# Optimization experiments

Measured on AMD Instinct MI355X. Metric: run time of the kernel, lower is better.

Reference implementation:

```python
import jax, jax.numpy as jnp
import numpy as np

N_NODES = 50000
N_EDGES = 800000
IN_DIM, HID_DIM, OUT_DIM = 128, 256, 64


def setup_inputs() -> dict:
    key = jax.random.key(0)
    k1, k2, k3, k4 = jax.random.split(key, 4)
    x = jax.random.normal(k1, (N_NODES, IN_DIM), dtype=jnp.float32)
    edge_index = jax.random.randint(k2, (2, N_EDGES), 0, N_NODES, dtype=jnp.int32)
    # Glorot-ish scaled weights
    W1 = jax.random.normal(k3, (IN_DIM, HID_DIM), dtype=jnp.float32) * (1.0 / np.sqrt(IN_DIM))
    W2 = jax.random.normal(k4, (HID_DIM, OUT_DIM), dtype=jnp.float32) * (1.0 / np.sqrt(HID_DIM))
    b1 = jnp.zeros((HID_DIM,), dtype=jnp.float32)
    b2 = jnp.zeros((OUT_DIM,), dtype=jnp.float32)
    return {"x": x, "edge_index": edge_index, "W1": W1, "b1": b1, "W2": W2, "b2": b2}


def _gcn_conv(x, src, dst, deg_inv_sqrt, W, b):
    # transform first (PyG GCNConv order), then edge-normalized scatter-add
    h = x @ W                                        # [N, D_out]
    norm = deg_inv_sqrt[src] * deg_inv_sqrt[dst]     # [E]
    msgs = h[src] * norm[:, None]                    # [E, D_out]
    agg = jax.ops.segment_sum(msgs, dst, num_segments=x.shape[0])
    return agg + b


def reference(x, edge_index, W1, b1, W2, b2):
    n = x.shape[0]
    loops = jnp.arange(n, dtype=edge_index.dtype)
    src = jnp.concatenate([edge_index[0], loops])    # add self-loops
    dst = jnp.concatenate([edge_index[1], loops])
    deg = jax.ops.segment_sum(jnp.ones_like(dst, dtype=x.dtype), dst, num_segments=n)
    deg_inv_sqrt = jnp.where(deg > 0, jax.lax.rsqrt(jnp.maximum(deg, 1e-12)), 0.0)
    h = jax.nn.relu(_gcn_conv(x, src, dst, deg_inv_sqrt, W1, b1))
    h = _gcn_conv(h, src, dst, deg_inv_sqrt, W2, b2)
    return jax.nn.log_softmax(h, axis=1)
```

## Files before the change

kernel.cpp:

```cpp
#include <hip/hip_runtime.h>
#include <hip/hip_bf16.h>
#include <math.h>

#define N_NODES 50000
#define N_EDGES 800000
#define IN_DIM 128
#define HID_DIM 256
#define OUT_DIM 64
#define NPART 196
#define CHUNK 2048
#define NPB ((N_EDGES + CHUNK - 1) / CHUNK)
#define PREPB (N_NODES * IN_DIM / 4 / 256)

typedef __attribute__((ext_vector_type(8))) short bf16x8;
typedef __attribute__((ext_vector_type(4))) short short4v;
typedef __attribute__((ext_vector_type(4))) float f32x4;

__device__ inline short f2bf(float f) {
    unsigned u = __float_as_uint(f);
    unsigned r = (u + 0x7fffu + ((u >> 16) & 1u)) >> 16;
    return (short)r;
}
__device__ inline float bf_lo(unsigned u) { return __uint_as_float(u << 16); }
__device__ inline float bf_hi(unsigned u) { return __uint_as_float(u & 0xffff0000u); }

__global__ void hist_kernel(const int* __restrict__ dst, int* __restrict__ cnt, int E) {
    int e = blockIdx.x * blockDim.x + threadIdx.x;
    if (e < E) atomicAdd(&cnt[dst[e]], 1);
}

__global__ __launch_bounds__(256) void scan_pack_kernel(const int* __restrict__ cnt,
                                                        int* __restrict__ offs,
                                                        float* __restrict__ dis,
                                                        int* __restrict__ gcnt,
                                                        int* __restrict__ coarseBase,
                                                        int* __restrict__ coarseCnt,
                                                        int* __restrict__ coarseCursor,
                                                        const float* __restrict__ W1,
                                                        const float* __restrict__ W2,
                                                        short* __restrict__ Bp1,
                                                        short* __restrict__ Bp2, int n) {
    if (blockIdx.x >= NPART) {
        int idx = (blockIdx.x - NPART) * 256 + threadIdx.x;
        const float* W; short* Bp; int N;
        const int T1 = (IN_DIM / 32) * (HID_DIM / 16) * 64;
        const int T2 = (HID_DIM / 32) * (OUT_DIM / 16) * 64;
        if (idx < T1) { W = W1; Bp = Bp1; N = HID_DIM; }
        else { idx -= T1; if (idx >= T2) return; W = W2; Bp = Bp2; N = OUT_DIM; }
        int lane = idx & 63;
        int frag = idx >> 6;
        int ntiles = N >> 4;
        int nt = frag % ntiles;
        int kt = frag / ntiles;
        int col = nt * 16 + (lane & 15);
        int krow = kt * 32 + (lane >> 4) * 8;
        bf16x8 pk;
        #pragma unroll
        for (int j = 0; j < 8; j++) pk[j] = f2bf(W[(size_t)(krow + j) * N + col]);
        *((bf16x8*)(Bp + (size_t)idx * 8)) = pk;
        return;
    }
    __shared__ int ws[4];
    __shared__ int base;
    int tid = threadIdx.x, lane = tid & 63, wid = tid >> 6;
    int i = blockIdx.x * 256 + tid;
    int v = (i < n) ? cnt[i] : 0;
    int s = v;
    #pragma unroll
    for (int off = 1; off < 64; off <<= 1) {
        int t = __shfl_up(s, off, 64);
        if (lane >= off) s += t;
    }
    if (lane == 63) ws[wid] = s;
    __syncthreads();
    int wp = 0;
    #pragma unroll
    for (int w = 0; w < 4; w++) wp += (w < wid) ? ws[w] : 0;
    int excl = s - v + wp;
    if (tid == 255) {
        int total = excl + v;
        int b = atomicAdd(gcnt, total);
        base = b;
        coarseBase[blockIdx.x] = b;
        coarseCnt[blockIdx.x] = total;
        coarseCursor[blockIdx.x] = b;
    }
    __syncthreads();
    if (i < n) {
        offs[i] = base + excl;
        dis[i] = rsqrtf((float)v + 1.0f);
    }
}

__global__ __launch_bounds__(256) void part1_prep_kernel(const int* __restrict__ src,
                                                         const int* __restrict__ dst,
                                                         int* __restrict__ coarseCursor,
                                                         uint2* __restrict__ sedge,
                                                         const float* __restrict__ x,
                                                         const float* __restrict__ dis,
                                                         short* __restrict__ xb, int E) {
    __shared__ int cnt_l[NPART];
    __shared__ int pref[NPART];
    __shared__ int gbase[NPART];
    __shared__ int ws4[4];
    __shared__ uint2 stage[CHUNK];
    int tid = threadIdx.x;
    if (blockIdx.x >= NPB) {
        int idx = (blockIdx.x - NPB) * 256 + tid;
        int node = idx >> 5;
        float dn = dis[node];
        float4 v = ((const float4*)x)[idx];
        short4v o = {f2bf(v.x * dn), f2bf(v.y * dn), f2bf(v.z * dn), f2bf(v.w * dn)};
        ((short4v*)xb)[idx] = o;
        return;
    }
    int e0 = blockIdx.x * CHUNK;
    if (tid < NPART) cnt_l[tid] = 0;
    __syncthreads();
    int es[CHUNK / 256], ed[CHUNK / 256];
    #pragma unroll
    for (int j = 0; j < CHUNK / 256; j++) {
        int e = e0 + j * 256 + tid;
        if (e < E) {
            es[j] = src[e]; ed[j] = dst[e];
            atomicAdd(&cnt_l[ed[j] >> 8], 1);
        } else ed[j] = -1;
    }
    __syncthreads();
    int lane = tid & 63, wid = tid >> 6;
    int v = (tid < NPART) ? cnt_l[tid] : 0;
    int s = v;
    #pragma unroll
    for (int off = 1; off < 64; off <<= 1) {
        int t = __shfl_up(s, off, 64);
        if (lane >= off) s += t;
    }
    if (lane == 63) ws4[wid] = s;
    __syncthreads();
    int wp = 0;
    #pragma unroll
    for (int w = 0; w < 4; w++) wp += (w < wid) ? ws4[w] : 0;
    int excl = s - v + wp;
    if (tid < NPART) pref[tid] = excl;
    __syncthreads();
    if (tid < NPART) cnt_l[tid] = excl;
    __syncthreads();
    #pragma unroll
    for (int j = 0; j < CHUNK / 256; j++) {
        if (ed[j] >= 0) {
            int c = ed[j] >> 8;
            int p = atomicAdd(&cnt_l[c], 1);
            stage[p] = make_uint2((unsigned)es[j], (unsigned)ed[j]);
        }
    }
    __syncthreads();
    if (tid < NPART) {
        int cl = cnt_l[tid] - pref[tid];
        gbase[tid] = (cl > 0) ? atomicAdd(&coarseCursor[tid], cl) : 0;
    }
    __syncthreads();
    int total = (e0 + CHUNK <= E) ? CHUNK : (E - e0);
    for (int i = tid; i < total; i += 256) {
        uint2 ev = stage[i];
        int c = (int)(ev.y >> 8);
        sedge[gbase[c] + (i - pref[c])] = ev;
    }
}

__global__ __launch_bounds__(256) void part2_kernel(const uint2* __restrict__ sedge,
                                                    const int* __restrict__ coarseBase,
                                                    const int* __restrict__ coarseCnt,
                                                    const int* __restrict__ offs,
                                                    int* __restrict__ ssrc, int n) {
    __shared__ int cur[256];
    int b = blockIdx.x;
    int node0 = b * 256;
    int tid = threadIdx.x;
    if (node0 + tid < n) cur[tid] = offs[node0 + tid];
    __syncthreads();
    int base = coarseBase[b], cb = coarseCnt[b];
    for (int i = tid; i < cb; i += 256) {
        uint2 ev = sedge[base + i];
        int pos = atomicAdd(&cur[ev.y & 255], 1);
        ssrc[pos] = (int)ev.x;
    }
}

__global__ void agg1_kernel(const short* __restrict__ xb, const int* __restrict__ ssrc,
                            const int* __restrict__ offs, const int* __restrict__ cnt,
                            const float* __restrict__ dis, short* __restrict__ aggx, int n) {
    int lane = threadIdx.x & 63;
    int node = blockIdx.x * (blockDim.x >> 6) + (threadIdx.x >> 6);
    if (node >= n) return;
    int grp = lane >> 4, l16 = lane & 15;
    int start = offs[node], c = cnt[node];
    float acc[8] = {};
    int j = grp;
    for (; j + 12 < c; j += 16) {
        int s0 = ssrc[start + j];
        int s1 = ssrc[start + j + 4];
        int s2 = ssrc[start + j + 8];
        int s3 = ssrc[start + j + 12];
        uint4 p0 = *((const uint4*)(xb + (size_t)s0 * IN_DIM + l16 * 8));
        uint4 p1 = *((const uint4*)(xb + (size_t)s1 * IN_DIM + l16 * 8));
        uint4 p2 = *((const uint4*)(xb + (size_t)s2 * IN_DIM + l16 * 8));
        uint4 p3 = *((const uint4*)(xb + (size_t)s3 * IN_DIM + l16 * 8));
        acc[0] += bf_lo(p0.x); acc[1] += bf_hi(p0.x); acc[2] += bf_lo(p0.y); acc[3] += bf_hi(p0.y);
        acc[4] += bf_lo(p0.z); acc[5] += bf_hi(p0.z); acc[6] += bf_lo(p0.w); acc[7] += bf_hi(p0.w);
        acc[0] += bf_lo(p1.x); acc[1] += bf_hi(p1.x); acc[2] += bf_lo(p1.y); acc[3] += bf_hi(p1.y);
        acc[4] += bf_lo(p1.z); acc[5] += bf_hi(p1.z); acc[6] += bf_lo(p1.w); acc[7] += bf_hi(p1.w);
        acc[0] += bf_lo(p2.x); acc[1] += bf_hi(p2.x); acc[2] += bf_lo(p2.y); acc[3] += bf_hi(p2.y);
        acc[4] += bf_lo(p2.z); acc[5] += bf_hi(p2.z); acc[6] += bf_lo(p2.w); acc[7] += bf_hi(p2.w);
        acc[0] += bf_lo(p3.x); acc[1] += bf_hi(p3.x); acc[2] += bf_lo(p3.y); acc[3] += bf_hi(p3.y);
        acc[4] += bf_lo(p3.z); acc[5] += bf_hi(p3.z); acc[6] += bf_lo(p3.w); acc[7] += bf_hi(p3.w);
    }
    for (; j < c; j += 4) {
        int s0 = ssrc[start + j];
        uint4 p0 = *((const uint4*)(xb + (size_t)s0 * IN_DIM + l16 * 8));
        acc[0] += bf_lo(p0.x); acc[1] += bf_hi(p0.x); acc[2] += bf_lo(p0.y); acc[3] += bf_hi(p0.y);
        acc[4] += bf_lo(p0.z); acc[5] += bf_hi(p0.z); acc[6] += bf_lo(p0.w); acc[7] += bf_hi(p0.w);
    }
    #pragma unroll
    for (int k = 0; k < 8; k++) {
        acc[k] += __shfl_xor(acc[k], 16, 64);
        acc[k] += __shfl_xor(acc[k], 32, 64);
    }
    if (grp == 0) {
        float dn = dis[node];
        uint4 pk = *((const uint4*)(xb + (size_t)node * IN_DIM + l16 * 8));
        acc[0] += bf_lo(pk.x); acc[1] += bf_hi(pk.x); acc[2] += bf_lo(pk.y); acc[3] += bf_hi(pk.y);
        acc[4] += bf_lo(pk.z); acc[5] += bf_hi(pk.z); acc[6] += bf_lo(pk.w); acc[7] += bf_hi(pk.w);
        bf16x8 o;
        #pragma unroll
        for (int k = 0; k < 8; k++) o[k] = f2bf(acc[k] * dn);
        *((bf16x8*)(aggx + (size_t)node * IN_DIM + l16 * 8)) = o;
    }
}

#define H1_STRIDE 264
__global__ __launch_bounds__(256) void gemm_fused_kernel(const short* __restrict__ A,
                                                         const short* __restrict__ Bp1,
                                                         const short* __restrict__ Bp2,
                                                         const float* __restrict__ b1,
                                                         const float* __restrict__ dis,
                                                         short* __restrict__ h2, int M) {
    __shared__ short lds_h1[4][16][H1_STRIDE];
    int lane = threadIdx.x & 63;
    int w = threadIdx.x >> 6;
    int rowBase = blockIdx.x * 64 + w * 16;
    int arow = rowBase + (lane & 15);
    int kseg = lane >> 4;
    int col0 = lane & 15;

    constexpr int NT1 = HID_DIM / 16;
    f32x4 acc1[NT1] = {};
    #pragma unroll
    for (int kt = 0; kt < IN_DIM / 32; kt++) {
        bf16x8 a = {};
        if (arow < M)
            a = *((const bf16x8*)(A + (size_t)arow * IN_DIM + kt * 32 + kseg * 8));
        #pragma unroll
        for (int nt = 0; nt < NT1; nt++) {
            bf16x8 b = *((const bf16x8*)(Bp1 + ((size_t)(kt * NT1 + nt) * 64 + lane) * 8));
            acc1[nt] = __builtin_amdgcn_mfma_f32_16x16x32_bf16(a, b, acc1[nt], 0, 0, 0);
        }
    }
    #pragma unroll
    for (int nt = 0; nt < NT1; nt++) {
        float bv = b1[nt * 16 + col0];
        #pragma unroll
        for (int i = 0; i < 4; i++) {
            float v = fmaxf(acc1[nt][i] + bv, 0.0f);
            lds_h1[w][kseg * 4 + i][nt * 16 + col0] = f2bf(v);
        }
    }
    constexpr int NT2 = OUT_DIM / 16;
    f32x4 acc2[NT2] = {};
    #pragma unroll
    for (int kt = 0; kt < HID_DIM / 32; kt++) {
        bf16x8 a = *((const bf16x8*)&lds_h1[w][lane & 15][kt * 32 + kseg * 8]);
        #pragma unroll
        for (int nt = 0; nt < NT2; nt++) {
            bf16x8 b = *((const bf16x8*)(Bp2 + ((size_t)(kt * NT2 + nt) * 64 + lane) * 8));
            acc2[nt] = __builtin_amdgcn_mfma_f32_16x16x32_bf16(a, b, acc2[nt], 0, 0, 0);
        }
    }
    #pragma unroll
    for (int i = 0; i < 4; i++) {
        int r = rowBase + kseg * 4 + i;
        if (r >= M) continue;
        float sc = dis[r];
        #pragma unroll
        for (int nt = 0; nt < NT2; nt++)
            h2[(size_t)r * OUT_DIM + nt * 16 + col0] = f2bf(acc2[nt][i] * sc);
    }
}

__global__ void agg2_kernel(const short* __restrict__ h2, const int* __restrict__ ssrc,
                            const int* __restrict__ offs, const int* __restrict__ cnt,
                            const float* __restrict__ dis, const float* __restrict__ b2,
                            float* __restrict__ out, int n) {
    int lane = threadIdx.x & 63;
    int node = blockIdx.x * (blockDim.x >> 6) + (threadIdx.x >> 6);
    if (node >= n) return;
    int grp = lane >> 4, l16 = lane & 15;
    int start = offs[node], c = cnt[node];
    float acc[4] = {};
    int j = grp;
    for (; j + 12 < c; j += 16) {
        int s0 = ssrc[start + j];
        int s1 = ssrc[start + j + 4];
        int s2 = ssrc[start + j + 8];
        int s3 = ssrc[start + j + 12];
        uint2 p0 = *((const uint2*)(h2 + (size_t)s0 * OUT_DIM + l16 * 4));
        uint2 p1 = *((const uint2*)(h2 + (size_t)s1 * OUT_DIM + l16 * 4));
        uint2 p2 = *((const uint2*)(h2 + (size_t)s2 * OUT_DIM + l16 * 4));
        uint2 p3 = *((const uint2*)(h2 + (size_t)s3 * OUT_DIM + l16 * 4));
        acc[0] += bf_lo(p0.x); acc[1] += bf_hi(p0.x); acc[2] += bf_lo(p0.y); acc[3] += bf_hi(p0.y);
        acc[0] += bf_lo(p1.x); acc[1] += bf_hi(p1.x); acc[2] += bf_lo(p1.y); acc[3] += bf_hi(p1.y);
        acc[0] += bf_lo(p2.x); acc[1] += bf_hi(p2.x); acc[2] += bf_lo(p2.y); acc[3] += bf_hi(p2.y);
        acc[0] += bf_lo(p3.x); acc[1] += bf_hi(p3.x); acc[2] += bf_lo(p3.y); acc[3] += bf_hi(p3.y);
    }
    for (; j < c; j += 4) {
        int s0 = ssrc[start + j];
        uint2 p0 = *((const uint2*)(h2 + (size_t)s0 * OUT_DIM + l16 * 4));
        acc[0] += bf_lo(p0.x); acc[1] += bf_hi(p0.x); acc[2] += bf_lo(p0.y); acc[3] += bf_hi(p0.y);
    }
    #pragma unroll
    for (int k = 0; k < 4; k++) {
        acc[k] += __shfl_xor(acc[k], 16, 64);
        acc[k] += __shfl_xor(acc[k], 32, 64);
    }
    float dn = dis[node];
    uint2 pv = *((const uint2*)(h2 + (size_t)node * OUT_DIM + l16 * 4));
    float4 bb = ((const float4*)b2)[l16];
    acc[0] = (acc[0] + bf_lo(pv.x)) * dn + bb.x;
    acc[1] = (acc[1] + bf_hi(pv.x)) * dn + bb.y;
    acc[2] = (acc[2] + bf_lo(pv.y)) * dn + bb.z;
    acc[3] = (acc[3] + bf_hi(pv.y)) * dn + bb.w;
    float m = fmaxf(fmaxf(acc[0], acc[1]), fmaxf(acc[2], acc[3]));
    #pragma unroll
    for (int off = 1; off < 16; off <<= 1) m = fmaxf(m, __shfl_xor(m, off, 64));
    float ex = expf(acc[0] - m) + expf(acc[1] - m) + expf(acc[2] - m) + expf(acc[3] - m);
    #pragma unroll
    for (int off = 1; off < 16; off <<= 1) ex += __shfl_xor(ex, off, 64);
    float ls = m + logf(ex);
    if (grp == 0) {
        float4 o = {acc[0] - ls, acc[1] - ls, acc[2] - ls, acc[3] - ls};
        ((float4*)(out + (size_t)node * OUT_DIM))[l16] = o;
    }
}

extern "C" void kernel_launch(void* const* d_in, const int* in_sizes, int n_in,
                              void* d_out, int out_size, void* d_ws, size_t ws_size,
                              hipStream_t stream) {
    const float* x  = (const float*)d_in[0];
    const int*   ei = (const int*)d_in[1];
    const float* W1 = (const float*)d_in[2];
    const float* b1 = (const float*)d_in[3];
    const float* W2 = (const float*)d_in[4];
    const float* b2 = (const float*)d_in[5];
    float* out = (float*)d_out;
    char* ws = (char*)d_ws;

    const int* srcp = ei;
    const int* dstp = ei + N_EDGES;

    int*   cnt    = (int*)(ws);
    int*   gcnt   = (int*)(ws + 200000);
    int*   offs   = (int*)(ws + 262144);
    float* dis    = (float*)(ws + 524288);
    int*   coarseBase   = (int*)(ws + 786432);
    int*   coarseCnt    = (int*)(ws + 787456);
    int*   coarseCursor = (int*)(ws + 788480);
    short* Bp1    = (short*)(ws + 1048576);
    short* Bp2    = (short*)(ws + 1114112);
    int*   ssrc   = (int*)(ws + 1179648);
    uint2* sedge  = (uint2*)(ws + 4456448);
    short* aggx   = (short*)(ws + 4456448);
    short* xb     = (short*)(ws + 17301504);
    short* h2     = (short*)(ws + 30146560);

    hipMemsetAsync(cnt, 0, 200004, stream);

    hist_kernel<<<(N_EDGES + 255) / 256, 256, 0, stream>>>(dstp, cnt, N_EDGES);
    scan_pack_kernel<<<NPART + 24, 256, 0, stream>>>(cnt, offs, dis, gcnt,
                                                     coarseBase, coarseCnt, coarseCursor,
                                                     W1, W2, Bp1, Bp2, N_NODES);
    part1_prep_kernel<<<NPB + PREPB, 256, 0, stream>>>(srcp, dstp, coarseCursor, sedge,
                                                       x, dis, xb, N_EDGES);
    part2_kernel<<<NPART, 256, 0, stream>>>(sedge, coarseBase, coarseCnt, offs, ssrc, N_NODES);

    agg1_kernel<<<(N_NODES + 3) / 4, 256, 0, stream>>>(xb, ssrc, offs, cnt, dis, aggx, N_NODES);
    gemm_fused_kernel<<<(N_NODES + 63) / 64, 256, 0, stream>>>(aggx, Bp1, Bp2, b1, dis,
                                                               h2, N_NODES);
    agg2_kernel<<<(N_NODES + 3) / 4, 256, 0, stream>>>(h2, ssrc, offs, cnt, dis, b2, out, N_NODES);
}
```

Baseline: 228.3 us.

## Drop global histogram pass; bucket edges into fixed-capacity coarse partitions

Removes the global degree histogram and scan kernels. Edges are bucketed straight into fixed-capacity (CAP) slots per 256-node partition, and part2 then computes per-node counts, offsets and degree norms locally. The x-to-bf16 scaling also moves into part2, which cuts two launches and a pass over dst. The risk is that a coarse partition holding more than CAP edges would overflow; random uniform inputs average about 4096 per partition, and the ssrc layout gains gaps.

```diff
diff --git a/kernel.cpp b/kernel.cpp
--- a/kernel.cpp
+++ b/kernel.cpp
@@ -8,9 +8,9 @@
 #define HID_DIM 256
 #define OUT_DIM 64
 #define NPART 196
+#define CAP 8192
 #define CHUNK 2048
 #define NPB ((N_EDGES + CHUNK - 1) / CHUNK)
-#define PREPB (N_NODES * IN_DIM / 4 / 256)
 
 typedef __attribute__((ext_vector_type(8))) short bf16x8;
 typedef __attribute__((ext_vector_type(4))) short short4v;
@@ -24,24 +24,22 @@
 __device__ inline float bf_lo(unsigned u) { return __uint_as_float(u << 16); }
 __device__ inline float bf_hi(unsigned u) { return __uint_as_float(u & 0xffff0000u); }
 
-__global__ void hist_kernel(const int* __restrict__ dst, int* __restrict__ cnt, int E) {
-    int e = blockIdx.x * blockDim.x + threadIdx.x;
-    if (e < E) atomicAdd(&cnt[dst[e]], 1);
-}
-
-__global__ __launch_bounds__(256) void scan_pack_kernel(const int* __restrict__ cnt,
-                                                        int* __restrict__ offs,
-                                                        float* __restrict__ dis,
-                                                        int* __restrict__ gcnt,
-                                                        int* __restrict__ coarseBase,
-                                                        int* __restrict__ coarseCnt,
-                                                        int* __restrict__ coarseCursor,
-                                                        const float* __restrict__ W1,
-                                                        const float* __restrict__ W2,
-                                                        short* __restrict__ Bp1,
-                                                        short* __restrict__ Bp2, int n) {
-    if (blockIdx.x >= NPART) {
-        int idx = (blockIdx.x - NPART) * 256 + threadIdx.x;
+__global__ __launch_bounds__(256) void part1_pack_kernel(const int* __restrict__ src,
+                                                         const int* __restrict__ dst,
+                                                         int* __restrict__ coarseCursor,
+                                                         uint2* __restrict__ sedge,
+                                                         const float* __restrict__ W1,
+                                                         const float* __restrict__ W2,
+                                                         short* __restrict__ Bp1,
+                                                         short* __restrict__ Bp2, int E) {
+    __shared__ int cnt_l[NPART];
+    __shared__ int pref[NPART];
+    __shared__ int gbase[NPART];
+    __shared__ int ws4[4];
+    __shared__ uint2 stage[CHUNK];
+    int tid = threadIdx.x;
+    if (blockIdx.x >= NPB) {
+        int idx = (blockIdx.x - NPB) * 256 + tid;
         const float* W; short* Bp; int N;
         const int T1 = (IN_DIM / 32) * (HID_DIM / 16) * 64;
         const int T2 = (HID_DIM / 32) * (OUT_DIM / 16) * 64;
@@ -60,60 +58,6 @@
         *((bf16x8*)(Bp + (size_t)idx * 8)) = pk;
         return;
     }
-    __shared__ int ws[4];
-    __shared__ int base;
-    int tid = threadIdx.x, lane = tid & 63, wid = tid >> 6;
-    int i = blockIdx.x * 256 + tid;
-    int v = (i < n) ? cnt[i] : 0;
-    int s = v;
-    #pragma unroll
-    for (int off = 1; off < 64; off <<= 1) {
-        int t = __shfl_up(s, off, 64);
-        if (lane >= off) s += t;
-    }
-    if (lane == 63) ws[wid] = s;
-    __syncthreads();
-    int wp = 0;
-    #pragma unroll
-    for (int w = 0; w < 4; w++) wp += (w < wid) ? ws[w] : 0;
-    int excl = s - v + wp;
-    if (tid == 255) {
-        int total = excl + v;
-        int b = atomicAdd(gcnt, total);
-        base = b;
-        coarseBase[blockIdx.x] = b;
-        coarseCnt[blockIdx.x] = total;
-        coarseCursor[blockIdx.x] = b;
-    }
-    __syncthreads();
-    if (i < n) {
-        offs[i] = base + excl;
-        dis[i] = rsqrtf((float)v + 1.0f);
-    }
-}
-
-__global__ __launch_bounds__(256) void part1_prep_kernel(const int* __restrict__ src,
-                                                         const int* __restrict__ dst,
-                                                         int* __restrict__ coarseCursor,
-                                                         uint2* __restrict__ sedge,
-                                                         const float* __restrict__ x,
-                                                         const float* __restrict__ dis,
-                                                         short* __restrict__ xb, int E) {
-    __shared__ int cnt_l[NPART];
-    __shared__ int pref[NPART];
-    __shared__ int gbase[NPART];
-    __shared__ int ws4[4];
-    __shared__ uint2 stage[CHUNK];
-    int tid = threadIdx.x;
-    if (blockIdx.x >= NPB) {
-        int idx = (blockIdx.x - NPB) * 256 + tid;
-        int node = idx >> 5;
-        float dn = dis[node];
-        float4 v = ((const float4*)x)[idx];
-        short4v o = {f2bf(v.x * dn), f2bf(v.y * dn), f2bf(v.z * dn), f2bf(v.w * dn)};
-        ((short4v*)xb)[idx] = o;
-        return;
-    }
     int e0 = blockIdx.x * CHUNK;
     if (tid < NPART) cnt_l[tid] = 0;
     __syncthreads();
@@ -156,7 +100,7 @@
     __syncthreads();
     if (tid < NPART) {
         int cl = cnt_l[tid] - pref[tid];
-        gbase[tid] = (cl > 0) ? atomicAdd(&coarseCursor[tid], cl) : 0;
+        gbase[tid] = (cl > 0) ? (tid * CAP + atomicAdd(&coarseCursor[tid], cl)) : 0;
     }
     __syncthreads();
     int total = (e0 + CHUNK <= E) ? CHUNK : (E - e0);
@@ -168,21 +112,65 @@
 }
 
 __global__ __launch_bounds__(256) void part2_kernel(const uint2* __restrict__ sedge,
-                                                    const int* __restrict__ coarseBase,
                                                     const int* __restrict__ coarseCnt,
-                                                    const int* __restrict__ offs,
-                                                    int* __restrict__ ssrc, int n) {
-    __shared__ int cur[256];
-    int b = blockIdx.x;
-    int node0 = b * 256;
-    int tid = threadIdx.x;
-    if (node0 + tid < n) cur[tid] = offs[node0 + tid];
-    __syncthreads();
-    int base = coarseBase[b], cb = coarseCnt[b];
+                                                    int* __restrict__ offs,
+                                                    int* __restrict__ cntg,
+                                                    float* __restrict__ dis,
+                                                    int* __restrict__ ssrc,
+                                                    const float* __restrict__ x,
+                                                    short* __restrict__ xb, int n) {
+    __shared__ int kcnt[256];
+    __shared__ int ws4[4];
+    __shared__ float sdis[256];
+    int b = blockIdx.x, tid = threadIdx.x;
+    int base = b * CAP;
+    int cb = coarseCnt[b];
+    kcnt[tid] = 0;
+    __syncthreads();
     for (int i = tid; i < cb; i += 256) {
         uint2 ev = sedge[base + i];
-        int pos = atomicAdd(&cur[ev.y & 255], 1);
+        atomicAdd(&kcnt[ev.y & 255], 1);
+    }
+    __syncthreads();
+    int v = kcnt[tid];
+    int lane = tid & 63, wid = tid >> 6;
+    int s = v;
+    #pragma unroll
+    for (int off = 1; off < 64; off <<= 1) {
+        int t = __shfl_up(s, off, 64);
+        if (lane >= off) s += t;
+    }
+    if (lane == 63) ws4[wid] = s;
+    __syncthreads();
+    int wp = 0;
+    #pragma unroll
+    for (int w = 0; w < 4; w++) wp += (w < wid) ? ws4[w] : 0;
+    int excl = s - v + wp;
+    int node = b * 256 + tid;
+    float dn = rsqrtf((float)v + 1.0f);
+    if (node < n) {
+        offs[node] = base + excl;
+        cntg[node] = v;
+        dis[node] = dn;
+    }
+    sdis[tid] = dn;
+    __syncthreads();
+    kcnt[tid] = base + excl;
+    __syncthreads();
+    for (int i = tid; i < cb; i += 256) {
+        uint2 ev = sedge[base + i];
+        int pos = atomicAdd(&kcnt[ev.y & 255], 1);
         ssrc[pos] = (int)ev.x;
+    }
+    int rlane = tid & 31, rgrp = tid >> 5;
+    for (int rb = 0; rb < 32; rb++) {
+        int row = rb * 8 + rgrp;
+        int nd = b * 256 + row;
+        if (nd >= n) break;
+        float d2 = sdis[row];
+        float4 vv = ((const float4*)(x + (size_t)nd * IN_DIM))[rlane];
+        short4v o = {f2bf(vv.x * d2), f2bf(vv.y * d2), f2bf(vv.z * d2), f2bf(vv.w * d2)};
+        *((short4v*)(xb + (size_t)nd * IN_DIM + rlane * 4)) = o;
     }
 }
 
@@ -366,33 +354,26 @@
     const int* srcp = ei;
     const int* dstp = ei + N_EDGES;
 
-    int*   cnt    = (int*)(ws);
-    int*   gcnt   = (int*)(ws + 200000);
-    int*   offs   = (int*)(ws + 262144);
+    int*   coarseCursor = (int*)(ws);
+    int*   offs   = (int*)(ws + 4096);
+    int*   cntg   = (int*)(ws + 262144);
     float* dis    = (float*)(ws + 524288);
-    int*   coarseBase   = (int*)(ws + 786432);
-    int*   coarseCnt    = (int*)(ws + 787456);
-    int*   coarseCursor = (int*)(ws + 788480);
-    short* Bp1    = (short*)(ws + 1048576);
-    short* Bp2    = (short*)(ws + 1114112);
-    int*   ssrc   = (int*)(ws + 1179648);
-    uint2* sedge  = (uint2*)(ws + 4456448);
-    short* aggx   = (short*)(ws + 4456448);
-    short* xb     = (short*)(ws + 17301504);
-    short* h2     = (short*)(ws + 30146560);
-
-    hipMemsetAsync(cnt, 0, 200004, stream);
-
-    hist_kernel<<<(N_EDGES + 255) / 256, 256, 0, stream>>>(dstp, cnt, N_EDGES);
-    scan_pack_kernel<<<NPART + 24, 256, 0, stream>>>(cnt, offs, dis, gcnt,
-                                                     coarseBase, coarseCnt, coarseCursor,
-                                                     W1, W2, Bp1, Bp2, N_NODES);
-    part1_prep_kernel<<<NPB + PREPB, 256, 0, stream>>>(srcp, dstp, coarseCursor, sedge,
-                                                       x, dis, xb, N_EDGES);
-    part2_kernel<<<NPART, 256, 0, stream>>>(sedge, coarseBase, coarseCnt, offs, ssrc, N_NODES);
-
-    agg1_kernel<<<(N_NODES + 3) / 4, 256, 0, stream>>>(xb, ssrc, offs, cnt, dis, aggx, N_NODES);
+    short* Bp1    = (short*)(ws + 786432);
+    short* Bp2    = (short*)(ws + 851968);
+    int*   ssrc   = (int*)(ws + 917504);
+    uint2* sedge  = (uint2*)(ws + 7340032);
+    short* aggx   = (short*)(ws + 7340032);
+    short* xb     = (short*)(ws + 20185088);
+    short* h2     = (short*)(ws + 32985088);
+
+    hipMemsetAsync(coarseCursor, 0, NPART * 4, stream);
+
+    part1_pack_kernel<<<NPB + 24, 256, 0, stream>>>(srcp, dstp, coarseCursor, sedge,
+                                                    W1, W2, Bp1, Bp2, N_EDGES);
+    part2_kernel<<<NPART, 256, 0, stream>>>(sedge, coarseCursor, offs, cntg, dis, ssrc,
+                                            x, xb, N_NODES);
+    agg1_kernel<<<(N_NODES + 3) / 4, 256, 0, stream>>>(xb, ssrc, offs, cntg, dis, aggx, N_NODES);
     gemm_fused_kernel<<<(N_NODES + 63) / 64, 256, 0, stream>>>(aggx, Bp1, Bp2, b1, dis,
                                                                h2, N_NODES);
-    agg2_kernel<<<(N_NODES + 3) / 4, 256, 0, stream>>>(h2, ssrc, offs, cnt, dis, b2, out, N_NODES);
-}
+    agg2_kernel<<<(N_NODES + 3) / 4, 256, 0, stream>>>(h2, ssrc, offs, cntg, dis, b2, out, N_NODES);
+}
```

Measured after the change: 206.2 us. -9.7%, faster.
